# Kernel optimization log

Measured on AMD Instinct MI355X. Metric: run time of the kernel, lower is better.

## Reference

```python
import jax, jax.numpy as jnp
import numpy as np

STRIDES = (8, 16, 32)
BINS = 16
NC = 80
ALPHA, GAMMA = 0.25, 2.0
W_CLS, W_IOU, W_DFL = 1.0, 7.5, 1.5
B, MAX_GT = 32, 32
EPS = 1e-7


def setup_inputs() -> dict:
    key = jax.random.key(0)
    k0, k1, k2, k3, k4, k5, k6 = jax.random.split(key, 7)
    p0 = jax.random.normal(k0, (B, 4 * BINS + NC, 80, 80), dtype=jnp.float32)
    p1 = jax.random.normal(k1, (B, 4 * BINS + NC, 40, 40), dtype=jnp.float32)
    p2 = jax.random.normal(k2, (B, 4 * BINS + NC, 20, 20), dtype=jnp.float32)
    # realistic xyxy boxes inside a 640x640 image
    c = jax.random.uniform(k3, (B, MAX_GT, 2), minval=60.0, maxval=580.0)
    wh = jax.random.uniform(k4, (B, MAX_GT, 2), minval=16.0, maxval=120.0)
    gt_bboxes = jnp.concatenate([c - wh / 2, c + wh / 2], axis=-1).astype(jnp.float32)
    gt_labels = jax.random.randint(k5, (B, MAX_GT), 0, NC, dtype=jnp.int32)
    raw = jax.random.randint(k6, (B, 8400), 0, 20 * MAX_GT, dtype=jnp.int32)
    matched_gt_inds = jnp.where(raw < MAX_GT, raw, -1)
    return {"p0": p0, "p1": p1, "p2": p2, "gt_bboxes": gt_bboxes,
            "gt_labels": gt_labels, "matched_gt_inds": matched_gt_inds}


def _decode_scale(p, stride):
    # p: [B, 4*BINS + NC, H, W]
    Bp, C, H, W = p.shape
    dfl = p[:, :4 * BINS].reshape(Bp, 4, BINS, H, W)
    cls = p[:, 4 * BINS:]
    # DFL decode: expectation of softmax over bins, scaled by stride
    prob = jax.nn.softmax(dfl, axis=2)
    proj = jnp.arange(BINS, dtype=p.dtype)
    dist = jnp.einsum('bkchw,c->bkhw', prob, proj) * stride  # [B,4,H,W] in pixels
    ys, xs = jnp.meshgrid(jnp.arange(H), jnp.arange(W), indexing='ij')
    cx = ((xs.astype(p.dtype)) + 0.5) * stride
    cy = ((ys.astype(p.dtype)) + 0.5) * stride
    boxes = jnp.stack([cx - dist[:, 0], cy - dist[:, 1],
                       cx + dist[:, 2], cy + dist[:, 3]], axis=-1).reshape(Bp, H * W, 4)
    cls_logits = cls.transpose(0, 2, 3, 1).reshape(Bp, H * W, NC)
    dfl_flat = dfl.transpose(0, 3, 4, 1, 2).reshape(Bp, H * W, 4, BINS)
    grid = jnp.stack([cx, cy], axis=-1).reshape(H * W, 2)
    smap = jnp.full((H * W,), stride, dtype=p.dtype)
    return cls_logits, dfl_flat, boxes, grid, smap


def reference(p0, p1, p2, gt_bboxes, gt_labels, matched_gt_inds):
    outs = [_decode_scale(p, s) for p, s in zip((p0, p1, p2), STRIDES)]
    scores = jnp.concatenate([o[0] for o in outs], axis=1)   # [B,N,NC]
    dfl = jnp.concatenate([o[1] for o in outs], axis=1)      # [B,N,4,BINS]
    pboxes = jnp.concatenate([o[2] for o in outs], axis=1)   # [B,N,4]
    grid = jnp.concatenate([o[3] for o in outs], axis=0)     # [N,2]
    smap = jnp.concatenate([o[4] for o in outs], axis=0)     # [N]

    pos = matched_gt_inds >= 0                               # [B,N]
    idx = jnp.where(pos, matched_gt_inds, 0)
    lbl = jnp.take_along_axis(gt_labels, idx, axis=1)        # [B,N]
    posf = pos.astype(scores.dtype)
    tgt_scores = jax.nn.one_hot(lbl, NC, dtype=scores.dtype) * posf[..., None]

    # sigmoid focal loss (stable BCE-with-logits)
    prob = jax.nn.sigmoid(scores)
    ce = jnp.maximum(scores, 0) - scores * tgt_scores + jnp.log1p(jnp.exp(-jnp.abs(scores)))
    p_t = prob * tgt_scores + (1 - prob) * (1 - tgt_scores)
    alpha_t = tgt_scores * ALPHA + (1 - tgt_scores) * (1 - ALPHA)
    cls_elem = alpha_t * (1.0 - p_t) ** GAMMA * ce
    num_pos = jnp.maximum(posf.sum(), 1.0)
    loss_cls = cls_elem.sum() / num_pos

    # gather matched GT boxes per anchor
    tboxes = jnp.take_along_axis(gt_bboxes, idx[..., None], axis=1)  # [B,N,4]
    gx, gy = grid[None, :, 0], grid[None, :, 1]
    l = jnp.clip(gx - tboxes[..., 0], 0.0)
    t = jnp.clip(gy - tboxes[..., 1], 0.0)
    r = jnp.clip(tboxes[..., 2] - gx, 0.0)
    b_ = jnp.clip(tboxes[..., 3] - gy, 0.0)
    dists = jnp.stack([l, t, r, b_], axis=-1) / smap[None, :, None]   # [B,N,4]
    tb = jnp.clip(dists, 0.0, BINS - 1 - 1e-6)
    lo = jnp.floor(tb).astype(jnp.int32)
    hi = jnp.minimum(lo + 1, BINS - 1)
    a = tb - lo.astype(tb.dtype)
    # soft two-bin DFL target (vectorized form of the scatter_add loop)
    tdist = (jax.nn.one_hot(lo, BINS, dtype=dfl.dtype) * (1.0 - a)[..., None]
             + jax.nn.one_hot(hi, BINS, dtype=dfl.dtype) * a[..., None])   # [B,N,4,BINS]
    logp = jax.nn.log_softmax(dfl, axis=-1)
    dfl_elem = -(tdist * logp).sum(-1)                                # [B,N,4]
    loss_dfl = (dfl_elem * posf[..., None]).sum() / (num_pos * 4.0)

    # IoU loss on positives
    ix1 = jnp.maximum(pboxes[..., 0], tboxes[..., 0])
    iy1 = jnp.maximum(pboxes[..., 1], tboxes[..., 1])
    ix2 = jnp.minimum(pboxes[..., 2], tboxes[..., 2])
    iy2 = jnp.minimum(pboxes[..., 3], tboxes[..., 3])
    inter = jnp.clip(ix2 - ix1, 0.0) * jnp.clip(iy2 - iy1, 0.0)
    area_p = jnp.clip(pboxes[..., 2] - pboxes[..., 0], 0.0) * jnp.clip(pboxes[..., 3] - pboxes[..., 1], 0.0)
    area_t = jnp.clip(tboxes[..., 2] - tboxes[..., 0], 0.0) * jnp.clip(tboxes[..., 3] - tboxes[..., 1], 0.0)
    iou = inter / (area_p + area_t - inter + EPS)
    loss_iou = ((1.0 - iou) * posf).sum() / num_pos

    total = W_CLS * loss_cls + W_IOU * loss_iou + W_DFL * loss_dfl
    return total
```

## Files before the change

### kernel.cpp

```cpp
#include <hip/hip_runtime.h>
#include <math.h>

#define NCLS 80
#define BINS 16
#define BATCH 32
#define MAX_GT 32
#define NA 8400
#define AN (BATCH * NA)
#define NT 2100
#define ALPHA_C 0.25f
#define W_CLS 1.0
#define W_IOU 7.5
#define W_DFL 1.5
#define EPS_F 1e-7f


__device__ __forceinline__ void scale_map(int t,
    const float* __restrict__ p0, const float* __restrict__ p1, const float* __restrict__ p2,
    const float*& p, int& HW, int& W, float& stride, int& off, int& gbase)
{
    if (t < 1600)      { p = p0; HW = 6400; W = 80; stride = 8.f;  off = t * 4;          gbase = 0;    }
    else if (t < 2000) { p = p1; HW = 1600; W = 40; stride = 16.f; off = (t - 1600) * 4; gbase = 6400; }
    else               { p = p2; HW = 400;  W = 20; stride = 32.f; off = (t - 2000) * 4; gbase = 8000; }
}

__device__ __forceinline__ void block_reduce_atomic(float val, double* __restrict__ target)
{
    __shared__ float s[4];
    __syncthreads();
    #pragma unroll
    for (int o = 32; o > 0; o >>= 1) val += __shfl_down(val, o);
    const int wave = threadIdx.x >> 6, lane = threadIdx.x & 63;
    if (lane == 0) s[wave] = val;
    __syncthreads();
    if (threadIdx.x == 0) atomicAdd(target, (double)(s[0] + s[1] + s[2] + s[3]));
}

__global__ __launch_bounds__(256) void yolo_dfl_cls(
    const float* __restrict__ p0, const float* __restrict__ p1, const float* __restrict__ p2,
    const float* __restrict__ gt_bboxes, const int* __restrict__ gt_labels,
    const int* __restrict__ matched, float* __restrict__ pdist, double* __restrict__ acc)
{
    const int t    = blockIdx.x * 256 + threadIdx.x;
    const int role = blockIdx.y;
    const int b    = blockIdx.z;

    float part = 0.f;

    if (role >= 4) {
        const int chq = role - 4;
        if (t < NT) {
            const float* p; int HW, W, off, gbase; float stride;
            scale_map(t, p0, p1, p2, p, HW, W, stride, off, gbase);

            const int4 m4 = *(const int4*)(matched + (size_t)b * NA + gbase + off);
            const int mm[4] = {m4.x, m4.y, m4.z, m4.w};
            int lbl[4];
            #pragma unroll
            for (int j = 0; j < 4; ++j)
                lbl[j] = (mm[j] >= 0) ? gt_labels[b * MAX_GT + mm[j]] : -1;

            const float* pcls = p + (size_t)(b * 144 + 4 * BINS + chq * 20) * (size_t)HW + (size_t)off;

            #pragma unroll 4
            for (int cc = 0; cc < 20; ++cc) {
                const int c = chq * 20 + cc;
                float4 q = *(const float4*)(pcls + (size_t)cc * HW);
                const float s4[4] = {q.x, q.y, q.z, q.w};
                #pragma unroll
                for (int j = 0; j < 4; ++j) {
                    float s  = s4[j];
                    float tt = (c == lbl[j]) ? 1.f : 0.f;
                    float e   = __expf(-fabsf(s));
                    float inv = 1.f / (1.f + e);
                    float prob = (s >= 0.f) ? inv : e * inv;
                    float ce  = fmaxf(s, 0.f) - s * tt + __logf(1.f + e);
                    float p_t = prob * tt + (1.f - prob) * (1.f - tt);
                    float alpha_t = tt * ALPHA_C + (1.f - tt) * (1.f - ALPHA_C);
                    float om = 1.f - p_t;
                    part += alpha_t * om * om * ce;
                }
            }
        }
        block_reduce_atomic(part, &acc[0]);
    } else {
        const int k = role;
        if (t < NT) {
            const float* p; int HW, W, off, gbase; float stride;
            scale_map(t, p0, p1, p2, p, HW, W, stride, off, gbase);
            const float inv_s = 1.f / stride;

            const int h  = off / W;
            const int w0 = off - h * W;
            const float cy = ((float)h + 0.5f) * stride;

            const int4 m4 = *(const int4*)(matched + (size_t)b * NA + gbase + off);
            const int mm[4] = {m4.x, m4.y, m4.z, m4.w};

            float tdv[4]; bool pos[4];
            #pragma unroll
            for (int j = 0; j < 4; ++j) {
                pos[j] = (mm[j] >= 0);
                int idx = pos[j] ? mm[j] : 0;
                float4 tb = *(const float4*)(gt_bboxes + ((size_t)b * MAX_GT + idx) * 4);
                float cx = ((float)(w0 + j) + 0.5f) * stride;
                float d;
                if      (k == 0) d = cx   - tb.x;
                else if (k == 1) d = cy   - tb.y;
                else if (k == 2) d = tb.z - cx;
                else             d = tb.w - cy;
                tdv[j] = fmaxf(d, 0.f) * inv_s;
            }

            const float* pc = p + (size_t)(b * 144 + k * BINS) * (size_t)HW + (size_t)off;
            float v[BINS][4];
            #pragma unroll
            for (int i = 0; i < BINS; ++i) {
                float4 q = *(const float4*)(pc + (size_t)i * HW);
                v[i][0] = q.x; v[i][1] = q.y; v[i][2] = q.z; v[i][3] = q.w;
            }

            float pd[4];
            #pragma unroll
            for (int j = 0; j < 4; ++j) {
                float tval = fminf(tdv[j], (float)(BINS - 1) - 1e-6f);
                int   lo = (int)floorf(tval);
                float fr = tval - (float)lo;

                float mx = v[0][j];
                #pragma unroll
                for (int i = 1; i < BINS; ++i) mx = fmaxf(mx, v[i][j]);

                float se = 0.f, we = 0.f, vlo = 0.f, vhi = 0.f;
                #pragma unroll
                for (int i = 0; i < BINS; ++i) {
                    float e = __expf(v[i][j] - mx);
                    se += e;
                    we += (float)i * e;
                    vlo = (i == lo)     ? v[i][j] : vlo;
                    vhi = (i == lo + 1) ? v[i][j] : vhi;
                }
                pd[j] = (we / se) * stride;
                if (pos[j]) {
                    float lse = mx + __logf(se);
                    part += -((1.f - fr) * (vlo - lse) + fr * (vhi - lse));
                }
            }
            float4 st = {pd[0], pd[1], pd[2], pd[3]};
            *(float4*)(pdist + (size_t)k * AN + (size_t)b * NA + gbase + off) = st;
        }
        block_reduce_atomic(part, &acc[2]);
    }
}

__global__ __launch_bounds__(256) void yolo_iou(
    const float* __restrict__ gt_bboxes, const int* __restrict__ matched,
    const float* __restrict__ pdist, double* __restrict__ acc)
{
    const int t = blockIdx.x * 256 + threadIdx.x;
    const int b = blockIdx.y;

    float iou_acc = 0.f, cnt = 0.f;

    if (t < NT) {
        const float* dummy; int HW, W, off, gbase; float stride;
        scale_map(t, dummy, dummy, dummy, dummy, HW, W, stride, off, gbase);

        const int h  = off / W;
        const int w0 = off - h * W;
        const float cy = ((float)h + 0.5f) * stride;

        const int4 m4 = *(const int4*)(matched + (size_t)b * NA + gbase + off);
        const int mm[4] = {m4.x, m4.y, m4.z, m4.w};

        float pdj[4][4];
        #pragma unroll
        for (int k = 0; k < 4; ++k) {
            float4 q = *(const float4*)(pdist + (size_t)k * AN + (size_t)b * NA + gbase + off);
            pdj[k][0] = q.x; pdj[k][1] = q.y; pdj[k][2] = q.z; pdj[k][3] = q.w;
        }

        #pragma unroll
        for (int j = 0; j < 4; ++j) {
            if (mm[j] >= 0) {
                float4 tb = *(const float4*)(gt_bboxes + ((size_t)b * MAX_GT + mm[j]) * 4);
                float cx = ((float)(w0 + j) + 0.5f) * stride;
                float px1 = cx - pdj[0][j], py1 = cy - pdj[1][j];
                float px2 = cx + pdj[2][j], py2 = cy + pdj[3][j];
                float ix1 = fmaxf(px1, tb.x), iy1 = fmaxf(py1, tb.y);
                float ix2 = fminf(px2, tb.z), iy2 = fminf(py2, tb.w);
                float inter  = fmaxf(ix2 - ix1, 0.f) * fmaxf(iy2 - iy1, 0.f);
                float area_p = fmaxf(px2 - px1, 0.f) * fmaxf(py2 - py1, 0.f);
                float area_t = fmaxf(tb.z - tb.x, 0.f) * fmaxf(tb.w - tb.y, 0.f);
                float iou = inter / (area_p + area_t - inter + EPS_F);
                iou_acc += 1.f - iou;
                cnt += 1.f;
            }
        }
    }
    block_reduce_atomic(iou_acc, &acc[1]);
    block_reduce_atomic(cnt,     &acc[3]);
}

__global__ __launch_bounds__(256) void yolo_loss_fused(
    const float* __restrict__ p0, const float* __restrict__ p1, const float* __restrict__ p2,
    const float* __restrict__ gt_bboxes, const int* __restrict__ gt_labels,
    const int* __restrict__ matched, double* __restrict__ acc)
{
    const int a = blockIdx.x * blockDim.x + threadIdx.x;
    const int b = blockIdx.y;
    float cls_acc = 0.f, iou_acc = 0.f, dfl_acc = 0.f;
    int pos_cnt = 0;
    if (a < NA) {
        const float* p; int HW, W; float stride; int off;
        if (a < 6400)      { p = p0; HW = 6400; W = 80; stride = 8.f;  off = a; }
        else if (a < 8000) { p = p1; HW = 1600; W = 40; stride = 16.f; off = a - 6400; }
        else               { p = p2; HW = 400;  W = 20; stride = 32.f; off = a - 8000; }
        const int h = off / W, w = off - h * W;
        const float cx = ((float)w + 0.5f) * stride, cy = ((float)h + 0.5f) * stride;
        const float* pb = p + ((size_t)b * 144) * (size_t)HW + (size_t)off;
        const int m = matched[(size_t)b * NA + a];
        const bool pos = (m >= 0);
        const int idx = pos ? m : 0;
        const int lbl = gt_labels[b * MAX_GT + idx];
        const float* tbp = gt_bboxes + ((size_t)b * MAX_GT + idx) * 4;
        const float tx1 = tbp[0], ty1 = tbp[1], tx2 = tbp[2], ty2 = tbp[3];
        float tdist[4] = {fmaxf(cx - tx1, 0.f) / stride, fmaxf(cy - ty1, 0.f) / stride,
                          fmaxf(tx2 - cx, 0.f) / stride, fmaxf(ty2 - cy, 0.f) / stride};
        float pdv[4]; float dfl_sum = 0.f;
        #pragma unroll
        for (int k = 0; k < 4; ++k) {
            float tv = fminf(tdist[k], (float)(BINS - 1) - 1e-6f);
            int lo = (int)floorf(tv);
            float fr = tv - (float)lo;
            const float* pc = pb + (size_t)(k * BINS) * HW;
            float v[BINS];
            #pragma unroll
            for (int i = 0; i < BINS; ++i) v[i] = pc[(size_t)i * HW];
            float mx = v[0];
            #pragma unroll
            for (int i = 1; i < BINS; ++i) mx = fmaxf(mx, v[i]);
            float se = 0.f, we = 0.f, vlo = 0.f, vhi = 0.f;
            #pragma unroll
            for (int i = 0; i < BINS; ++i) {
                float e = __expf(v[i] - mx);
                se += e; we += (float)i * e;
                vlo = (i == lo) ? v[i] : vlo;
                vhi = (i == lo + 1) ? v[i] : vhi;
            }
            pdv[k] = (we / se) * stride;
            if (pos) { float lse = mx + __logf(se); dfl_sum += -((1.f - fr) * (vlo - lse) + fr * (vhi - lse)); }
        }
        const float* pcls = pb + (size_t)(4 * BINS) * HW;
        #pragma unroll 4
        for (int c = 0; c < NCLS; ++c) {
            float s = pcls[(size_t)c * HW];
            float tt = (pos && c == lbl) ? 1.f : 0.f;
            float e = __expf(-fabsf(s));
            float inv = 1.f / (1.f + e);
            float prob = (s >= 0.f) ? inv : e * inv;
            float ce = fmaxf(s, 0.f) - s * tt + __logf(1.f + e);
            float p_t = prob * tt + (1.f - prob) * (1.f - tt);
            float alpha_t = tt * ALPHA_C + (1.f - tt) * (1.f - ALPHA_C);
            float om = 1.f - p_t;
            cls_acc += alpha_t * om * om * ce;
        }
        if (pos) {
            float px1 = cx - pdv[0], py1 = cy - pdv[1], px2 = cx + pdv[2], py2 = cy + pdv[3];
            float ix1 = fmaxf(px1, tx1), iy1 = fmaxf(py1, ty1);
            float ix2 = fminf(px2, tx2), iy2 = fminf(py2, ty2);
            float inter  = fmaxf(ix2 - ix1, 0.f) * fmaxf(iy2 - iy1, 0.f);
            float area_p = fmaxf(px2 - px1, 0.f) * fmaxf(py2 - py1, 0.f);
            float area_t = fmaxf(tx2 - tx1, 0.f) * fmaxf(ty2 - ty1, 0.f);
            float iou = inter / (area_p + area_t - inter + EPS_F);
            iou_acc = 1.f - iou; dfl_acc = dfl_sum; pos_cnt = 1;
        }
    }
    #pragma unroll
    for (int o = 32; o > 0; o >>= 1) {
        cls_acc += __shfl_down(cls_acc, o);
        iou_acc += __shfl_down(iou_acc, o);
        dfl_acc += __shfl_down(dfl_acc, o);
        pos_cnt += __shfl_down(pos_cnt, o);
    }
    __shared__ float sc[4], si[4], sd[4]; __shared__ int sn[4];
    const int wave = threadIdx.x >> 6, lane = threadIdx.x & 63;
    if (lane == 0) { sc[wave] = cls_acc; si[wave] = iou_acc; sd[wave] = dfl_acc; sn[wave] = pos_cnt; }
    __syncthreads();
    if (threadIdx.x == 0) {
        atomicAdd(&acc[0], (double)(sc[0]+sc[1]+sc[2]+sc[3]));
        atomicAdd(&acc[1], (double)(si[0]+si[1]+si[2]+si[3]));
        atomicAdd(&acc[2], (double)(sd[0]+sd[1]+sd[2]+sd[3]));
        atomicAdd(&acc[3], (double)(sn[0]+sn[1]+sn[2]+sn[3]));
    }
}

__global__ void yolo_loss_finalize(const double* __restrict__ acc, float* __restrict__ out)
{
    double np = acc[3] < 1.0 ? 1.0 : acc[3];
    double total = W_CLS * acc[0] / np + W_IOU * acc[1] / np + W_DFL * acc[2] / (np * 4.0);
    out[0] = (float)total;
}

extern "C" void kernel_launch(void* const* d_in, const int* in_sizes, int n_in,
                              void* d_out, int out_size, void* d_ws, size_t ws_size,
                              hipStream_t stream)
{
    const float* p0        = (const float*)d_in[0];
    const float* p1        = (const float*)d_in[1];
    const float* p2        = (const float*)d_in[2];
    const float* gt_bboxes = (const float*)d_in[3];
    const int*   gt_labels = (const int*)d_in[4];
    const int*   matched   = (const int*)d_in[5];
    float*  out   = (float*)d_out;
    double* acc   = (double*)d_ws;
    float*  pdist = (float*)((char*)d_ws + 256);

    (void)hipMemsetAsync(acc, 0, 4 * sizeof(double), stream);

    const size_t need = 256 + (size_t)4 * AN * sizeof(float);
    if (ws_size >= need) {
        dim3 g1((NT + 255) / 256, 8, BATCH);
        yolo_dfl_cls<<<g1, 256, 0, stream>>>(p0, p1, p2, gt_bboxes, gt_labels, matched, pdist, acc);
        dim3 g2((NT + 255) / 256, BATCH);
        yolo_iou<<<g2, 256, 0, stream>>>(gt_bboxes, matched, pdist, acc);
    } else {
        dim3 g((NA + 255) / 256, BATCH);
        yolo_loss_fused<<<g, 256, 0, stream>>>(p0, p1, p2, gt_bboxes, gt_labels, matched, acc);
    }
    yolo_loss_finalize<<<1, 1, 0, stream>>>(acc, out);
}
```

Baseline: 226.3 us.

## Restructure cls/DFL work into per-plane blocks with precomputed label map and slotted atomics

Result: no change. 229.4 us (+1.4%).

```diff
diff --git a/kernel.cpp b/kernel.cpp
--- a/kernel.cpp
+++ b/kernel.cpp
@@ -8,21 +8,16 @@
 #define NA 8400
 #define AN (BATCH * NA)
 #define NT 2100
+#define NB_CLS 5120
+#define NB_DFL 525
+#define DFL_THREADS (NB_DFL * 256)
+#define NSLOT 64
 #define ALPHA_C 0.25f
 #define W_CLS 1.0
 #define W_IOU 7.5
 #define W_DFL 1.5
 #define EPS_F 1e-7f
 
-
-__device__ __forceinline__ void scale_map(int t,
-    const float* __restrict__ p0, const float* __restrict__ p1, const float* __restrict__ p2,
-    const float*& p, int& HW, int& W, float& stride, int& off, int& gbase)
-{
-    if (t < 1600)      { p = p0; HW = 6400; W = 80; stride = 8.f;  off = t * 4;          gbase = 0;    }
-    else if (t < 2000) { p = p1; HW = 1600; W = 40; stride = 16.f; off = (t - 1600) * 4; gbase = 6400; }
-    else               { p = p2; HW = 400;  W = 20; stride = 32.f; off = (t - 2000) * 4; gbase = 8000; }
-}
 
 __device__ __forceinline__ void block_reduce_atomic(float val, double* __restrict__ target)
 {
@@ -36,62 +31,82 @@
     if (threadIdx.x == 0) atomicAdd(target, (double)(s[0] + s[1] + s[2] + s[3]));
 }
 
-__global__ __launch_bounds__(256) void yolo_dfl_cls(
+__global__ __launch_bounds__(256) void yolo_prep(
+    const int* __restrict__ matched, const int* __restrict__ gt_labels,
+    signed char* __restrict__ lblmap)
+{
+    const int qid = blockIdx.x * 256 + threadIdx.x;
+    if (qid >= AN / 4) return;
+    const int a0 = qid * 4;
+    const int b  = a0 / NA;
+    const int4 m4 = *(const int4*)(matched + a0);
+    const int mm[4] = {m4.x, m4.y, m4.z, m4.w};
+    char4 o;
+    o.x = (mm[0] >= 0) ? (signed char)gt_labels[b * MAX_GT + mm[0]] : (signed char)-1;
+    o.y = (mm[1] >= 0) ? (signed char)gt_labels[b * MAX_GT + mm[1]] : (signed char)-1;
+    o.z = (mm[2] >= 0) ? (signed char)gt_labels[b * MAX_GT + mm[2]] : (signed char)-1;
+    o.w = (mm[3] >= 0) ? (signed char)gt_labels[b * MAX_GT + mm[3]] : (signed char)-1;
+    *(char4*)(lblmap + a0) = o;
+}
+
+__global__ __launch_bounds__(256) void yolo_mega(
     const float* __restrict__ p0, const float* __restrict__ p1, const float* __restrict__ p2,
-    const float* __restrict__ gt_bboxes, const int* __restrict__ gt_labels,
-    const int* __restrict__ matched, float* __restrict__ pdist, double* __restrict__ acc)
-{
-    const int t    = blockIdx.x * 256 + threadIdx.x;
-    const int role = blockIdx.y;
-    const int b    = blockIdx.z;
-
+    const float* __restrict__ gt_bboxes, const int* __restrict__ matched,
+    const signed char* __restrict__ lblmap,
+    float* __restrict__ pdist, double* __restrict__ acc)
+{
+    const int bid  = blockIdx.x;
+    const int slot = bid & (NSLOT - 1);
     float part = 0.f;
 
-    if (role >= 4) {
-        const int chq = role - 4;
-        if (t < NT) {
-            const float* p; int HW, W, off, gbase; float stride;
-            scale_map(t, p0, p1, p2, p, HW, W, stride, off, gbase);
-
-            const int4 m4 = *(const int4*)(matched + (size_t)b * NA + gbase + off);
-            const int mm[4] = {m4.x, m4.y, m4.z, m4.w};
-            int lbl[4];
-            #pragma unroll
-            for (int j = 0; j < 4; ++j)
-                lbl[j] = (mm[j] >= 0) ? gt_labels[b * MAX_GT + mm[j]] : -1;
-
-            const float* pcls = p + (size_t)(b * 144 + 4 * BINS + chq * 20) * (size_t)HW + (size_t)off;
-
-            #pragma unroll 4
-            for (int cc = 0; cc < 20; ++cc) {
-                const int c = chq * 20 + cc;
-                float4 q = *(const float4*)(pcls + (size_t)cc * HW);
-                const float s4[4] = {q.x, q.y, q.z, q.w};
-                #pragma unroll
-                for (int j = 0; j < 4; ++j) {
-                    float s  = s4[j];
-                    float tt = (c == lbl[j]) ? 1.f : 0.f;
-                    float e   = __expf(-fabsf(s));
-                    float inv = 1.f / (1.f + e);
-                    float prob = (s >= 0.f) ? inv : e * inv;
-                    float ce  = fmaxf(s, 0.f) - s * tt + __logf(1.f + e);
-                    float p_t = prob * tt + (1.f - prob) * (1.f - tt);
-                    float alpha_t = tt * ALPHA_C + (1.f - tt) * (1.f - ALPHA_C);
-                    float om = 1.f - p_t;
-                    part += alpha_t * om * om * ce;
-                }
-            }
-        }
-        block_reduce_atomic(part, &acc[0]);
+    if (bid < NB_CLS) {
+        const int plane = bid >> 1;
+        const int b = plane / NCLS;
+        const int c = plane - b * NCLS;
+
+        for (int t = (bid & 1) * 256 + (int)threadIdx.x; t < NT; t += 512) {
+            const float* p; int HW, off, gbase;
+            if (t < 1600)      { p = p0; HW = 6400; off = t * 4;          gbase = 0;    }
+            else if (t < 2000) { p = p1; HW = 1600; off = (t - 1600) * 4; gbase = 6400; }
+            else               { p = p2; HW = 400;  off = (t - 2000) * 4; gbase = 8000; }
+
+            float4 q = *(const float4*)(p + (size_t)(b * 144 + 4 * BINS + c) * HW + off);
+            char4 l4 = *(const char4*)(lblmap + b * NA + gbase + off);
+            const int   lbl[4] = {l4.x, l4.y, l4.z, l4.w};
+            const float s4[4]  = {q.x, q.y, q.z, q.w};
+            #pragma unroll
+            for (int j = 0; j < 4; ++j) {
+                float s  = s4[j];
+                float tt = (c == lbl[j]) ? 1.f : 0.f;
+                float e   = __expf(-fabsf(s));
+                float inv = 1.f / (1.f + e);
+                float prob = (s >= 0.f) ? inv : e * inv;
+                float ce  = fmaxf(s, 0.f) - s * tt + __logf(1.f + e);
+                float p_t = prob * tt + (1.f - prob) * (1.f - tt);
+                float alpha_t = tt * ALPHA_C + (1.f - tt) * (1.f - ALPHA_C);
+                float om = 1.f - p_t;
+                part += alpha_t * om * om * ce;
+            }
+        }
+        block_reduce_atomic(part, &acc[0 * NSLOT + slot]);
     } else {
-        const int k = role;
-        if (t < NT) {
-            const float* p; int HW, W, off, gbase; float stride;
-            scale_map(t, p0, p1, p2, p, HW, W, stride, off, gbase);
+        const int dt0 = (bid - NB_CLS) * 256 + (int)threadIdx.x;
+        #pragma unroll
+        for (int rep = 0; rep < 2; ++rep) {
+            const int it = dt0 + rep * DFL_THREADS;
+            const int t  = it % NT;
+            const int r  = it / NT;
+            const int b  = r & 31;
+            const int k  = r >> 5;
+
+            const float* p; int HW, off, gbase, h, w0; float stride;
+            if (t < 1600)      { p = p0; HW = 6400; off = t * 4;          gbase = 0;    stride = 8.f;
+                                 h = t / 20;  w0 = (t - h * 20) * 4; }
+            else if (t < 2000) { p = p1; HW = 1600; off = (t - 1600) * 4; gbase = 6400; stride = 16.f;
+                                 int u = t - 1600; h = u / 10; w0 = (u - h * 10) * 4; }
+            else               { p = p2; HW = 400;  off = (t - 2000) * 4; gbase = 8000; stride = 32.f;
+                                 int u = t - 2000; h = u / 5;  w0 = (u - h * 5) * 4; }
             const float inv_s = 1.f / stride;
-
-            const int h  = off / W;
-            const int w0 = off - h * W;
             const float cy = ((float)h + 0.5f) * stride;
 
             const int4 m4 = *(const int4*)(matched + (size_t)b * NA + gbase + off);
@@ -104,15 +119,12 @@
                 int idx = pos[j] ? mm[j] : 0;
                 float4 tb = *(const float4*)(gt_bboxes + ((size_t)b * MAX_GT + idx) * 4);
                 float cx = ((float)(w0 + j) + 0.5f) * stride;
-                float d;
-                if      (k == 0) d = cx   - tb.x;
-                else if (k == 1) d = cy   - tb.y;
-                else if (k == 2) d = tb.z - cx;
-                else             d = tb.w - cy;
+                float d = (k == 0) ? (cx - tb.x) : (k == 1) ? (cy - tb.y)
+                        : (k == 2) ? (tb.z - cx) : (tb.w - cy);
                 tdv[j] = fmaxf(d, 0.f) * inv_s;
             }
 
-            const float* pc = p + (size_t)(b * 144 + k * BINS) * (size_t)HW + (size_t)off;
+            const float* pc = p + (size_t)(b * 144 + k * BINS) * HW + off;
             float v[BINS][4];
             #pragma unroll
             for (int i = 0; i < BINS; ++i) {
@@ -149,7 +161,7 @@
             float4 st = {pd[0], pd[1], pd[2], pd[3]};
             *(float4*)(pdist + (size_t)k * AN + (size_t)b * NA + gbase + off) = st;
         }
-        block_reduce_atomic(part, &acc[2]);
+        block_reduce_atomic(part, &acc[2 * NSLOT + slot]);
     }
 }
 
@@ -159,12 +171,15 @@
 {
     const int t = blockIdx.x * 256 + threadIdx.x;
     const int b = blockIdx.y;
+    const int slot = (blockIdx.x + blockIdx.y * 9) & (NSLOT - 1);
 
     float iou_acc = 0.f, cnt = 0.f;
 
     if (t < NT) {
-        const float* dummy; int HW, W, off, gbase; float stride;
-        scale_map(t, dummy, dummy, dummy, dummy, HW, W, stride, off, gbase);
+        int HW, W, off, gbase; float stride;
+        if (t < 1600)      { HW = 6400; W = 80; stride = 8.f;  off = t * 4;          gbase = 0;    }
+        else if (t < 2000) { HW = 1600; W = 40; stride = 16.f; off = (t - 1600) * 4; gbase = 6400; }
+        else               { HW = 400;  W = 20; stride = 32.f; off = (t - 2000) * 4; gbase = 8000; }
 
         const int h  = off / W;
         const int w0 = off - h * W;
@@ -198,8 +213,8 @@
             }
         }
     }
-    block_reduce_atomic(iou_acc, &acc[1]);
-    block_reduce_atomic(cnt,     &acc[3]);
+    block_reduce_atomic(iou_acc, &acc[1 * NSLOT + slot]);
+    block_reduce_atomic(cnt,     &acc[3 * NSLOT + slot]);
 }
 
 __global__ __launch_bounds__(256) void yolo_loss_fused(
@@ -209,8 +224,8 @@
 {
     const int a = blockIdx.x * blockDim.x + threadIdx.x;
     const int b = blockIdx.y;
-    float cls_acc = 0.f, iou_acc = 0.f, dfl_acc = 0.f;
-    int pos_cnt = 0;
+    const int slot = blockIdx.x & (NSLOT - 1);
+    float cls_acc = 0.f, iou_acc = 0.f, dfl_acc = 0.f, pos_cnt = 0.f;
     if (a < NA) {
         const float* p; int HW, W; float stride; int off;
         if (a < 6400)      { p = p0; HW = 6400; W = 80; stride = 8.f;  off = a; }
@@ -273,32 +288,22 @@
             float area_p = fmaxf(px2 - px1, 0.f) * fmaxf(py2 - py1, 0.f);
             float area_t = fmaxf(tx2 - tx1, 0.f) * fmaxf(ty2 - ty1, 0.f);
             float iou = inter / (area_p + area_t - inter + EPS_F);
-            iou_acc = 1.f - iou; dfl_acc = dfl_sum; pos_cnt = 1;
+            iou_acc = 1.f - iou; dfl_acc = dfl_sum; pos_cnt = 1.f;
         }
     }
-    #pragma unroll
-    for (int o = 32; o > 0; o >>= 1) {
-        cls_acc += __shfl_down(cls_acc, o);
-        iou_acc += __shfl_down(iou_acc, o);
-        dfl_acc += __shfl_down(dfl_acc, o);
-        pos_cnt += __shfl_down(pos_cnt, o);
-    }
-    __shared__ float sc[4], si[4], sd[4]; __shared__ int sn[4];
-    const int wave = threadIdx.x >> 6, lane = threadIdx.x & 63;
-    if (lane == 0) { sc[wave] = cls_acc; si[wave] = iou_acc; sd[wave] = dfl_acc; sn[wave] = pos_cnt; }
-    __syncthreads();
-    if (threadIdx.x == 0) {
-        atomicAdd(&acc[0], (double)(sc[0]+sc[1]+sc[2]+sc[3]));
-        atomicAdd(&acc[1], (double)(si[0]+si[1]+si[2]+si[3]));
-        atomicAdd(&acc[2], (double)(sd[0]+sd[1]+sd[2]+sd[3]));
-        atomicAdd(&acc[3], (double)(sn[0]+sn[1]+sn[2]+sn[3]));
-    }
+    block_reduce_atomic(cls_acc, &acc[0 * NSLOT + slot]);
+    block_reduce_atomic(iou_acc, &acc[1 * NSLOT + slot]);
+    block_reduce_atomic(dfl_acc, &acc[2 * NSLOT + slot]);
+    block_reduce_atomic(pos_cnt, &acc[3 * NSLOT + slot]);
 }
 
 __global__ void yolo_loss_finalize(const double* __restrict__ acc, float* __restrict__ out)
 {
-    double np = acc[3] < 1.0 ? 1.0 : acc[3];
-    double total = W_CLS * acc[0] / np + W_IOU * acc[1] / np + W_DFL * acc[2] / (np * 4.0);
+    double s[4] = {0.0, 0.0, 0.0, 0.0};
+    for (int q = 0; q < 4; ++q)
+        for (int i = 0; i < NSLOT; ++i) s[q] += acc[q * NSLOT + i];
+    double np = s[3] < 1.0 ? 1.0 : s[3];
+    double total = W_CLS * s[0] / np + W_IOU * s[1] / np + W_DFL * s[2] / (np * 4.0);
     out[0] = (float)total;
 }
 
@@ -312,16 +317,21 @@
     const float* gt_bboxes = (const float*)d_in[3];
     const int*   gt_labels = (const int*)d_in[4];
     const int*   matched   = (const int*)d_in[5];
-    float*  out   = (float*)d_out;
-    double* acc   = (double*)d_ws;
-    float*  pdist = (float*)((char*)d_ws + 256);
-
-    (void)hipMemsetAsync(acc, 0, 4 * sizeof(double), stream);
-
-    const size_t need = 256 + (size_t)4 * AN * sizeof(float);
+    float*  out = (float*)d_out;
+
+    const size_t accBytes   = 4 * NSLOT * sizeof(double);
+    const size_t pdistBytes = (size_t)4 * AN * sizeof(float);
+    double*      acc    = (double*)d_ws;
+    float*       pdist  = (float*)((char*)d_ws + accBytes);
+    signed char* lblmap = (signed char*)((char*)d_ws + accBytes + pdistBytes);
+    const size_t need = accBytes + pdistBytes + (size_t)AN;
+
+    (void)hipMemsetAsync(acc, 0, accBytes, stream);
+
     if (ws_size >= need) {
-        dim3 g1((NT + 255) / 256, 8, BATCH);
-        yolo_dfl_cls<<<g1, 256, 0, stream>>>(p0, p1, p2, gt_bboxes, gt_labels, matched, pdist, acc);
+        yolo_prep<<<(AN / 4 + 255) / 256, 256, 0, stream>>>(matched, gt_labels, lblmap);
+        yolo_mega<<<NB_CLS + NB_DFL, 256, 0, stream>>>(p0, p1, p2, gt_bboxes, matched,
+                                                       lblmap, pdist, acc);
         dim3 g2((NT + 255) / 256, BATCH);
         yolo_iou<<<g2, 256, 0, stream>>>(gt_bboxes, matched, pdist, acc);
     } else {
```
